# Performance work log

Measured on AMD Instinct MI355X. Metric: run time of the kernel, lower is better.

Reference implementation:

```python
import jax, jax.numpy as jnp
import numpy as np

NUM_CLASSES = 64
CDF_DIM = 128
EMBED_DIM = 1024
BATCH = 16


def setup_inputs() -> dict:
    key = jax.random.key(0)
    k_x, k_w1, k_b1, k_w2, k_b2 = jax.random.split(key, 5)
    bound1 = 1.0 / np.sqrt(EMBED_DIM)
    x = jax.random.normal(k_x, (BATCH, NUM_CLASSES * CDF_DIM, EMBED_DIM), dtype=jnp.float32)
    # stacked per-class weights: W1 [C,E,E] (applied as x @ W1), b1 [C,E], W2 [C,E], b2 [C]
    W1 = jax.random.uniform(k_w1, (NUM_CLASSES, EMBED_DIM, EMBED_DIM), jnp.float32, -bound1, bound1)
    b1 = jax.random.uniform(k_b1, (NUM_CLASSES, EMBED_DIM), jnp.float32, -bound1, bound1)
    W2 = jax.random.uniform(k_w2, (NUM_CLASSES, EMBED_DIM), jnp.float32, -bound1, bound1)
    b2 = jax.random.uniform(k_b2, (NUM_CLASSES,), jnp.float32, -bound1, bound1)
    return {"x": x, "W1": W1, "b1": b1, "W2": W2, "b2": b2}


def reference(x, W1, b1, W2, b2):
    B = x.shape[0]
    # [B, C, T, E] where T = cdf_dim
    xr = x.reshape(B, NUM_CLASSES, CDF_DIM, EMBED_DIM)
    # per-class first Linear + exact GELU (torch default is erf-based)
    h = jnp.einsum('bcte,ceo->bcto', xr, W1) + b1[None, :, None, :]
    h = jax.nn.gelu(h, approximate=False)
    # per-class second Linear to scalar, squeeze
    out = jnp.einsum('bcte,ce->bct', h, W2) + b2[None, :, None]
    # concat over classes -> [B, C*T]
    return out.reshape(B, NUM_CLASSES * CDF_DIM)
```

## Files before the change

### kernel.cpp

```cpp
#include <hip/hip_runtime.h>
#include <hip/hip_bf16.h>
#include <math.h>

#define NCLS 64
#define TDIM 128
#define EMB  1024
#define NBATCH 16

#define BM 128
#define BN 128
#define BK 32

typedef __attribute__((ext_vector_type(8))) short bfrag8;
typedef __attribute__((ext_vector_type(4))) float ffrag4;

__device__ __forceinline__ unsigned int pk2(float lo, float hi) {
    union { __hip_bfloat162 h; unsigned int u; } cv;
    cv.h = __float22bfloat162_rn(make_float2(lo, hi));
    return cv.u;
}
__device__ __forceinline__ short f2bs(float f) {
    return (short)(pk2(f, 0.f) & 0xffff);
}

union S8 { bfrag8 s; unsigned int u[4]; };

__device__ __forceinline__ void async16(const short* g, const short* l) {
    __builtin_amdgcn_global_load_lds(
        (const __attribute__((address_space(1))) unsigned int*)(unsigned long long)(uintptr_t)g,
        (__attribute__((address_space(3))) unsigned int*)(unsigned int)(uintptr_t)l,
        16, 0, 0);
}

__global__ __launch_bounds__(256) void init_out(const float* __restrict__ b2,
                                                float* __restrict__ out) {
    int i = blockIdx.x * 256 + threadIdx.x;
    int c = (i >> 7) & (NCLS - 1);
    out[i] = b2[c];
}

__global__ __launch_bounds__(256) void cvt_x(const float* __restrict__ x,
                                             short* __restrict__ xb) {
    size_t i = ((size_t)blockIdx.x * 256 + threadIdx.x) * 8;
    float4 a = *(const float4*)(x + i);
    float4 b = *(const float4*)(x + i + 4);
    S8 p;
    p.u[0] = pk2(a.x, a.y); p.u[1] = pk2(a.z, a.w);
    p.u[2] = pk2(b.x, b.y); p.u[3] = pk2(b.z, b.w);
    *(bfrag8*)(xb + i) = p.s;
}

__global__ __launch_bounds__(256) void cvt_w1t(const float* __restrict__ W1,
                                               short* __restrict__ w1t) {
    const int bid = blockIdx.x;
    const int nt = bid & 15, kt = (bid >> 4) & 15, c = bid >> 8;
    const int t = threadIdx.x;
    __shared__ short ldsT[64 * 72];

    const float* src = W1 + (size_t)c * 1048576 + (size_t)(kt * 64) * 1024 + nt * 64;
    const int kr = t >> 4, nq = (t & 15) * 4;
#pragma unroll
    for (int i = 0; i < 4; ++i) {
        int k = kr + i * 16;
        float4 v = *(const float4*)(src + (size_t)k * 1024 + nq);
        ldsT[(nq + 0) * 72 + k] = f2bs(v.x);
        ldsT[(nq + 1) * 72 + k] = f2bs(v.y);
        ldsT[(nq + 2) * 72 + k] = f2bs(v.z);
        ldsT[(nq + 3) * 72 + k] = f2bs(v.w);
    }
    __syncthreads();
    short* dst = w1t + (size_t)c * 1048576 + (size_t)(nt * 64) * 1024 + kt * 64;
#pragma unroll
    for (int p = 0; p < 2; ++p) {
        int chunk = t + p * 256;
        int n = chunk >> 3, kc = chunk & 7;
        bfrag8 v = *(const bfrag8*)(ldsT + n * 72 + kc * 8);
        *(bfrag8*)(dst + (size_t)n * 1024 + kc * 8) = v;
    }
}

__global__ __launch_bounds__(256) void mlp_gemm(
    const short* __restrict__ xb, const short* __restrict__ w1t,
    const float* __restrict__ b1, const float* __restrict__ W2,
    float* __restrict__ out)
{
    const int bid = blockIdx.x;
    const int nb = bid & 7;
    const int mb = (bid >> 3) & 15;
    const int c  = bid >> 7;

    __shared__ __align__(16) short lds_a[BM * BK];
    __shared__ __align__(16) short lds_b[BN * BK];

    const int tid  = threadIdx.x;
    const int lane = tid & 63;
    const int wave = tid >> 6;
    const int wm = wave >> 1, wn = wave & 1;
    const int quad = lane >> 4, l16 = lane & 15;

    const short* gA0 = xb + ((size_t)mb * 8192 + c * 128 + (2 * wave) * 16 + l16) * 1024
                          + quad * 8;
    const short* gA1 = gA0 + 16 * 1024;
    const short* gB0 = w1t + (size_t)c * 1048576
                           + (size_t)(nb * 128 + (2 * wave) * 16 + l16) * 1024 + quad * 8;
    const short* gB1 = gB0 + 16 * 1024;
    const short* lA0 = lds_a + (2 * wave) * 512;
    const short* lA1 = lA0 + 512;
    const short* lB0 = lds_b + (2 * wave) * 512;
    const short* lB1 = lB0 + 512;

    const short* ard = lds_a + (wm * 4) * 512 + quad * 128 + l16 * 8;
    const short* brd = lds_b + (wn * 4) * 512 + quad * 128 + l16 * 8;

    ffrag4 acc[4][4] = {};

    for (int kt = 0; kt < EMB / BK; ++kt) {
        __syncthreads();
        async16(gA0, lA0);
        async16(gA1, lA1);
        async16(gB0, lB0);
        async16(gB1, lB1);
        gA0 += BK; gA1 += BK; gB0 += BK; gB1 += BK;
        __syncthreads();

        bfrag8 af[4], bf[4];
#pragma unroll
        for (int mi = 0; mi < 4; ++mi) af[mi] = *(const bfrag8*)(ard + mi * 512);
#pragma unroll
        for (int ni = 0; ni < 4; ++ni) bf[ni] = *(const bfrag8*)(brd + ni * 512);
#pragma unroll
        for (int mi = 0; mi < 4; ++mi)
#pragma unroll
            for (int ni = 0; ni < 4; ++ni)
                acc[mi][ni] = __builtin_amdgcn_mfma_f32_16x16x32_bf16(
                    af[mi], bf[ni], acc[mi][ni], 0, 0, 0);
    }

    const int nbase = c * 1024 + nb * 128 + wn * 64 + l16;
    float b1v[4], w2v[4];
#pragma unroll
    for (int ni = 0; ni < 4; ++ni) {
        b1v[ni] = b1[nbase + ni * 16];
        w2v[ni] = W2[nbase + ni * 16];
    }

    float* outp = out + (size_t)mb * 8192 + c * 128 + wm * 64 + quad * 4;
#pragma unroll
    for (int mi = 0; mi < 4; ++mi) {
        float s[4] = {0.f, 0.f, 0.f, 0.f};
#pragma unroll
        for (int ni = 0; ni < 4; ++ni) {
#pragma unroll
            for (int r = 0; r < 4; ++r) {
                float h = acc[mi][ni][r] + b1v[ni];
                float g = 0.5f * h * (1.0f + erff(h * 0.70710678118654752f));
                s[r] += g * w2v[ni];
            }
        }
#pragma unroll
        for (int r = 0; r < 4; ++r) {
            s[r] += __shfl_xor(s[r], 8, 64);
            s[r] += __shfl_xor(s[r], 4, 64);
            s[r] += __shfl_xor(s[r], 2, 64);
            s[r] += __shfl_xor(s[r], 1, 64);
            if (l16 == 0) atomicAdd(outp + mi * 16 + r, s[r]);
        }
    }
}

__global__ __launch_bounds__(256) void mlp_head_fallback(
    const float* __restrict__ x,  const float* __restrict__ W1,
    const float* __restrict__ b1, const float* __restrict__ W2,
    float* __restrict__ out)
{
    const int bid = blockIdx.x;
    const int nb = bid & 7;
    const int mb = (bid >> 3) & 15;
    const int c  = bid >> 7;

    __shared__ __align__(16) short lds_a[BM * BK];
    __shared__ __align__(16) short lds_b[BN * BK];

    const int tid  = threadIdx.x;
    const int lane = tid & 63;
    const int wave = tid >> 6;
    const int wm = wave >> 1, wn = wave & 1;
    const int quad = lane >> 4, l16 = lane & 15;

    const int arow = tid & 127;
    const int akh  = tid >> 7;
    const float* aptr = x + ((size_t)mb * 8192 + (size_t)c * 128 + arow) * 1024 + akh * 16;
    short* aw0 = lds_a + (arow >> 4) * 512 + (akh * 2) * 128 + (arow & 15) * 8;
    short* aw1 = aw0 + 128;

    const int ncol = tid & 127;
    const int bkh  = tid >> 7;
    const float* bptr = W1 + (size_t)c * 1024 * 1024 + (size_t)(bkh * 16) * 1024
                           + (size_t)nb * 128 + ncol;
    short* bw0 = lds_b + (ncol >> 4) * 512 + (bkh * 2) * 128 + (ncol & 15) * 8;
    short* bw1 = bw0 + 128;

    const short* ard = lds_a + (wm * 4) * 512 + quad * 128 + l16 * 8;
    const short* brd = lds_b + (wn * 4) * 512 + quad * 128 + l16 * 8;

    ffrag4 acc[4][4] = {};

    for (int kt = 0; kt < EMB / BK; ++kt) {
        float4 a0 = *(const float4*)(aptr + 0);
        float4 a1 = *(const float4*)(aptr + 4);
        float4 a2 = *(const float4*)(aptr + 8);
        float4 a3 = *(const float4*)(aptr + 12);
        float bv[16];
#pragma unroll
        for (int j = 0; j < 16; ++j) bv[j] = bptr[(size_t)j * 1024];
        aptr += BK;
        bptr += (size_t)BK * 1024;

        __syncthreads();

        S8 pa0, pa1, pb0, pb1;
        pa0.u[0] = pk2(a0.x, a0.y); pa0.u[1] = pk2(a0.z, a0.w);
        pa0.u[2] = pk2(a1.x, a1.y); pa0.u[3] = pk2(a1.z, a1.w);
        pa1.u[0] = pk2(a2.x, a2.y); pa1.u[1] = pk2(a2.z, a2.w);
        pa1.u[2] = pk2(a3.x, a3.y); pa1.u[3] = pk2(a3.z, a3.w);
#pragma unroll
        for (int j = 0; j < 4; ++j) pb0.u[j] = pk2(bv[2 * j], bv[2 * j + 1]);
#pragma unroll
        for (int j = 0; j < 4; ++j) pb1.u[j] = pk2(bv[8 + 2 * j], bv[9 + 2 * j]);

        *(bfrag8*)aw0 = pa0.s;
        *(bfrag8*)aw1 = pa1.s;
        *(bfrag8*)bw0 = pb0.s;
        *(bfrag8*)bw1 = pb1.s;

        __syncthreads();

        bfrag8 af[4], bf[4];
#pragma unroll
        for (int mi = 0; mi < 4; ++mi) af[mi] = *(const bfrag8*)(ard + mi * 512);
#pragma unroll
        for (int ni = 0; ni < 4; ++ni) bf[ni] = *(const bfrag8*)(brd + ni * 512);
#pragma unroll
        for (int mi = 0; mi < 4; ++mi)
#pragma unroll
            for (int ni = 0; ni < 4; ++ni)
                acc[mi][ni] = __builtin_amdgcn_mfma_f32_16x16x32_bf16(
                    af[mi], bf[ni], acc[mi][ni], 0, 0, 0);
    }

    const int nbase = c * 1024 + nb * 128 + wn * 64 + l16;
    float b1v[4], w2v[4];
#pragma unroll
    for (int ni = 0; ni < 4; ++ni) {
        b1v[ni] = b1[nbase + ni * 16];
        w2v[ni] = W2[nbase + ni * 16];
    }

    float* outp = out + (size_t)mb * 8192 + c * 128 + wm * 64 + quad * 4;
#pragma unroll
    for (int mi = 0; mi < 4; ++mi) {
        float s[4] = {0.f, 0.f, 0.f, 0.f};
#pragma unroll
        for (int ni = 0; ni < 4; ++ni) {
#pragma unroll
            for (int r = 0; r < 4; ++r) {
                float h = acc[mi][ni][r] + b1v[ni];
                float g = 0.5f * h * (1.0f + erff(h * 0.70710678118654752f));
                s[r] += g * w2v[ni];
            }
        }
#pragma unroll
        for (int r = 0; r < 4; ++r) {
            s[r] += __shfl_xor(s[r], 8, 64);
            s[r] += __shfl_xor(s[r], 4, 64);
            s[r] += __shfl_xor(s[r], 2, 64);
            s[r] += __shfl_xor(s[r], 1, 64);
            if (l16 == 0) atomicAdd(outp + mi * 16 + r, s[r]);
        }
    }
}

extern "C" void kernel_launch(void* const* d_in, const int* in_sizes, int n_in,
                              void* d_out, int out_size, void* d_ws, size_t ws_size,
                              hipStream_t stream) {
    const float* x  = (const float*)d_in[0];
    const float* W1 = (const float*)d_in[1];
    const float* b1 = (const float*)d_in[2];
    const float* W2 = (const float*)d_in[3];
    const float* b2 = (const float*)d_in[4];
    float* out = (float*)d_out;

    const size_t xb_bytes  = (size_t)NBATCH * NCLS * TDIM * EMB * 2;
    const size_t w1t_bytes = (size_t)NCLS * EMB * EMB * 2;

    init_out<<<dim3(512), dim3(256), 0, stream>>>(b2, out);

    if (ws_size >= xb_bytes + w1t_bytes) {
        short* xb  = (short*)d_ws;
        short* w1t = (short*)((char*)d_ws + xb_bytes);
        cvt_x<<<dim3(65536), dim3(256), 0, stream>>>(x, xb);
        cvt_w1t<<<dim3(16384), dim3(256), 0, stream>>>(W1, w1t);
        mlp_gemm<<<dim3(NCLS * 16 * 8), dim3(256), 0, stream>>>(xb, w1t, b1, W2, out);
    } else {
        mlp_head_fallback<<<dim3(NCLS * 16 * 8), dim3(256), 0, stream>>>(x, W1, b1, W2, out);
    }
}
```

Before: 1.617 ms.

## Double-buffer LDS tiles and remap blocks so each class stays on one XCD

Adds a second LDS buffer for the A and B tiles. The next K-slice's async global-to-LDS loads are issued before the MFMAs on the current slice, and one barrier per iteration replaces two. This is meant to overlap memory latency with compute. The block index is also remapped so all 128 tiles of a class share the same XCD (bid & 7), which improves L2 reuse of that class's W1 slice. In exchange, LDS use per block doubles, which can lower occupancy.

```diff
diff --git a/kernel.cpp b/kernel.cpp
--- a/kernel.cpp
+++ b/kernel.cpp
@@ -85,12 +85,15 @@
     float* __restrict__ out)
 {
     const int bid = blockIdx.x;
-    const int nb = bid & 7;
-    const int mb = (bid >> 3) & 15;
-    const int c  = bid >> 7;
-
-    __shared__ __align__(16) short lds_a[BM * BK];
-    __shared__ __align__(16) short lds_b[BN * BK];
+    const int xcd = bid & 7;
+    const int idx = bid >> 3;
+    const int c   = ((idx >> 7) << 3) | xcd;
+    const int w   = idx & 127;
+    const int mb  = w >> 3;
+    const int nb  = w & 7;
+
+    __shared__ __align__(16) short lds_a[2 * BM * BK];
+    __shared__ __align__(16) short lds_b[2 * BN * BK];
 
     const int tid  = threadIdx.x;
     const int lane = tid & 63;
@@ -104,25 +107,34 @@
     const short* gB0 = w1t + (size_t)c * 1048576
                            + (size_t)(nb * 128 + (2 * wave) * 16 + l16) * 1024 + quad * 8;
     const short* gB1 = gB0 + 16 * 1024;
-    const short* lA0 = lds_a + (2 * wave) * 512;
-    const short* lA1 = lA0 + 512;
-    const short* lB0 = lds_b + (2 * wave) * 512;
-    const short* lB1 = lB0 + 512;
-
-    const short* ard = lds_a + (wm * 4) * 512 + quad * 128 + l16 * 8;
-    const short* brd = lds_b + (wn * 4) * 512 + quad * 128 + l16 * 8;
+    const int stA = (2 * wave) * 512;
 
     ffrag4 acc[4][4] = {};
 
+    async16(gA0, lds_a + stA);
+    async16(gA1, lds_a + stA + 512);
+    async16(gB0, lds_b + stA);
+    async16(gB1, lds_b + stA + 512);
+    gA0 += BK; gA1 += BK; gB0 += BK; gB1 += BK;
+    __syncthreads();
+
+    int cur = 0;
     for (int kt = 0; kt < EMB / BK; ++kt) {
-        __syncthreads();
-        async16(gA0, lA0);
-        async16(gA1, lA1);
-        async16(gB0, lB0);
-        async16(gB1, lB1);
-        gA0 += BK; gA1 += BK; gB0 += BK; gB1 += BK;
-        __syncthreads();
-
+        const short* la = lds_a + cur * (BM * BK);
+        const short* lb = lds_b + cur * (BN * BK);
+
+        if (kt + 1 < EMB / BK) {
+            short* na = (short*)(lds_a + (cur ^ 1) * (BM * BK) + stA);
+            short* nbp = (short*)(lds_b + (cur ^ 1) * (BN * BK) + stA);
+            async16(gA0, na);
+            async16(gA1, na + 512);
+            async16(gB0, nbp);
+            async16(gB1, nbp + 512);
+            gA0 += BK; gA1 += BK; gB0 += BK; gB1 += BK;
+        }
+
+        const short* ard = la + (wm * 4) * 512 + quad * 128 + l16 * 8;
+        const short* brd = lb + (wn * 4) * 512 + quad * 128 + l16 * 8;
         bfrag8 af[4], bf[4];
 #pragma unroll
         for (int mi = 0; mi < 4; ++mi) af[mi] = *(const bfrag8*)(ard + mi * 512);
@@ -134,6 +146,9 @@
             for (int ni = 0; ni < 4; ++ni)
                 acc[mi][ni] = __builtin_amdgcn_mfma_f32_16x16x32_bf16(
                     af[mi], bf[ni], acc[mi][ni], 0, 0, 0);
+
+        __syncthreads();
+        cur ^= 1;
     }
 
     const int nbase = c * 1024 + nb * 128 + wn * 64 + l16;
```

Result: faster. 1.509 ms (-6.7%).
